# Kernel optimization log

Hardware: AMD Instinct MI355X
Metric: run time of the kernel (lower is better)

Reference implementation:

```python
import jax, jax.numpy as jnp
import numpy as np

B, L = 512, 61440
E_MAX = 128          # max events per window (padded)
THRESHOLD = 0.5      # prob -> binary threshold
IOU_THR = 0.2        # IoU match threshold
LEN_THR = 128        # int(freq*time) = int(256*0.5)


def setup_inputs() -> dict:
    key = jax.random.key(0)
    k1, k2 = jax.random.split(key)
    # block-structured signals -> realistic long, sparse events
    out_blocks = jax.random.uniform(k1, (B, L // 256), dtype=jnp.float32)
    output = jnp.repeat(out_blocks, 256, axis=1)            # [B, L] probs
    tgt_blocks = (jax.random.uniform(k2, (B, L // 512)) > 0.75).astype(jnp.float32)
    target = jnp.repeat(tgt_blocks, 512, axis=1)            # [B, L] binary
    return {"output": output, "target": target}


def _filter_short(b):
    # zero out runs of ones shorter than LEN_THR (ProcessingPostEvent)
    starts = jnp.concatenate([b[:1], ((b[1:] - b[:-1]) == 1).astype(b.dtype)])
    run_id = jnp.cumsum(starts)                              # [L]
    run_len = jax.ops.segment_sum(b, run_id, num_segments=L + 1)
    return b * (run_len[run_id] >= LEN_THR).astype(b.dtype)


def _events(b):
    # binary_to_array: [start, end) pairs, padded to E_MAX with [L, L]
    padded = jnp.concatenate([jnp.zeros(1, b.dtype), b, jnp.zeros(1, b.dtype)])
    d = padded[1:] - padded[:-1]                             # [L+1]
    pos = jnp.arange(L + 1)
    starts = jnp.sort(jnp.where(d == 1, pos, L + 1))[:E_MAX]
    ends = jnp.sort(jnp.where(d == -1, pos, L + 1))[:E_MAX]
    starts = jnp.minimum(starts, L)
    ends = jnp.minimum(ends, L)
    n = (d == 1).sum()
    return starts, ends, n


def _best_match(iou):
    # iou: [E_MAX, E_MAX], invalid entries = -1
    max_col = iou.max(0); idx_col = iou.argmax(0)            # best output row per target col
    max_row = iou.max(1); idx_row = iou.argmax(1)            # best target col per output row
    ar = jnp.arange(E_MAX)
    mutual_row = (idx_col[idx_row] == ar) & (max_row >= IOU_THR)   # [E] rows in mutual match
    mutual_col = (idx_row[idx_col] == ar) & (max_col >= IOU_THR)   # [E] cols in mutual match
    row_one = (~mutual_row) & (max_row >= IOU_THR)
    col_one = (~mutual_col) & (max_col >= IOU_THR)
    onehot_row = (ar[None, :] == idx_row[:, None])           # bm[i, idx_row[i]]
    onehot_col = (ar[:, None] == idx_col[None, :])           # bm[idx_col[j], j]
    ones_m = (onehot_row & row_one[:, None]) | (onehot_col & col_one[None, :])
    kill = mutual_row[:, None] | mutual_col[None, :]         # rows/cols of mutual matches zeroed
    ones_m = ones_m & (~kill)
    tp = mutual_row.sum()                                    # count of '2' marks
    return tp, ones_m


def _per_batch(out_prob, tgt):
    b_out = _filter_short((out_prob >= THRESHOLD).astype(jnp.int32))
    b_tgt = (tgt != 0).astype(jnp.int32)
    s_o, e_o, n_out = _events(b_out)
    s_t, e_t, n_tgt = _events(b_tgt)
    inter = jnp.clip(jnp.minimum(e_o[:, None], e_t[None, :])
                     - jnp.maximum(s_o[:, None], s_t[None, :]), 0)
    la = (e_o - s_o)[:, None]
    lb = (e_t - s_t)[None, :]
    den = jnp.maximum(la + lb - inter, 1)
    valid = (jnp.arange(E_MAX) < n_out)[:, None] & (jnp.arange(E_MAX) < n_tgt)[None, :]
    iou = jnp.where(valid, inter.astype(jnp.float32) / den.astype(jnp.float32), -1.0)
    tp1, ones_m = _best_match(iou)
    # second pass on positions marked '1' (iou elsewhere zeroed in original)
    tp2, _ = _best_match(jnp.where(ones_m, iou, -1.0))
    tp = tp1 + tp2
    t_empty = n_tgt == 0
    o_empty = (~t_empty) & (n_out == 0)
    tp_b = jnp.where(t_empty | o_empty, 0, tp)
    # note: faithful to original (adds output count to FN when target empty, etc.)
    fn_b = jnp.where(t_empty, n_out, jnp.where(o_empty, 0, n_tgt - tp))
    fp_b = jnp.where(t_empty, 0, jnp.where(o_empty, n_tgt, n_out - tp))
    return tp_b, fn_b, fp_b


def reference(output, target):
    tp, fn, fp = jax.vmap(_per_batch)(output, target)
    TP = tp.sum().astype(jnp.float32)
    FN = fn.sum().astype(jnp.float32)
    FP = fp.sum().astype(jnp.float32)
    recall = jnp.where(TP + FN == 0, 0.0, TP / jnp.maximum(TP + FN, 1.0))
    precision = jnp.where(TP + FP == 0, 0.0, TP / jnp.maximum(TP + FP, 1.0))
    f1 = jnp.where(precision + recall == 0, 0.0,
                   2.0 * precision * recall / jnp.maximum(precision + recall, 1e-30))
    return recall, precision, f1
```

## Files before the change

kernel.cpp:

```cpp
#include <hip/hip_runtime.h>

typedef unsigned long long ull;

#define L_LEN 61440
#define NBATCH 512
#define EMAX 128
#define RUNBUF 128
#define NWORDS 960
#define NPADW 1080
#define PADW(w) ((w) + ((w) >> 3))
#define NTHREADS 512
#define IOU_THRESH 0.2f
#define LEN_THRESH 128
#define PADPK 0xF000F000u

__device__ __forceinline__ unsigned int mask16_ge(float4 a, float4 b, float4 c, float4 d, float thr) {
    unsigned int m = 0;
    m |= (a.x >= thr) ? 0x0001u : 0u; m |= (a.y >= thr) ? 0x0002u : 0u;
    m |= (a.z >= thr) ? 0x0004u : 0u; m |= (a.w >= thr) ? 0x0008u : 0u;
    m |= (b.x >= thr) ? 0x0010u : 0u; m |= (b.y >= thr) ? 0x0020u : 0u;
    m |= (b.z >= thr) ? 0x0040u : 0u; m |= (b.w >= thr) ? 0x0080u : 0u;
    m |= (c.x >= thr) ? 0x0100u : 0u; m |= (c.y >= thr) ? 0x0200u : 0u;
    m |= (c.z >= thr) ? 0x0400u : 0u; m |= (c.w >= thr) ? 0x0800u : 0u;
    m |= (d.x >= thr) ? 0x1000u : 0u; m |= (d.y >= thr) ? 0x2000u : 0u;
    m |= (d.z >= thr) ? 0x4000u : 0u; m |= (d.w >= thr) ? 0x8000u : 0u;
    return m;
}

__device__ __forceinline__ unsigned int mask16_ne0(float4 a, float4 b, float4 c, float4 d) {
    unsigned int m = 0;
    m |= (a.x != 0.0f) ? 0x0001u : 0u; m |= (a.y != 0.0f) ? 0x0002u : 0u;
    m |= (a.z != 0.0f) ? 0x0004u : 0u; m |= (a.w != 0.0f) ? 0x0008u : 0u;
    m |= (b.x != 0.0f) ? 0x0010u : 0u; m |= (b.y != 0.0f) ? 0x0020u : 0u;
    m |= (b.z != 0.0f) ? 0x0040u : 0u; m |= (b.w != 0.0f) ? 0x0080u : 0u;
    m |= (c.x != 0.0f) ? 0x0100u : 0u; m |= (c.y != 0.0f) ? 0x0200u : 0u;
    m |= (c.z != 0.0f) ? 0x0400u : 0u; m |= (c.w != 0.0f) ? 0x0800u : 0u;
    m |= (d.x != 0.0f) ? 0x1000u : 0u; m |= (d.y != 0.0f) ? 0x2000u : 0u;
    m |= (d.z != 0.0f) ? 0x4000u : 0u; m |= (d.w != 0.0f) ? 0x8000u : 0u;
    return m;
}

__device__ __forceinline__ float iou_pk(unsigned int pk, int ms, int me, int ml) {
    int s = (int)(pk & 0xffffu), e = (int)(pk >> 16);
    int lo = me < e ? me : e;
    int hi = ms > s ? ms : s;
    int inter = lo - hi; if (inter < 0) inter = 0;
    int den = ml + (e - s) - inter; if (den < 1) den = 1;
    return (float)inter / (float)den;
}

__global__ __launch_bounds__(NTHREADS) void event_f1_kernel(
        const float* __restrict__ outp, const float* __restrict__ tgtp,
        int* __restrict__ counters) {
    __shared__ ull bm[2][NPADW];
    __shared__ int runs_s[2][RUNBUF], runs_e[2][RUNBUF];
    __shared__ int wtot_s[8], wtot_e[8];
    __shared__ __align__(16) unsigned int pse_o[EMAX], pse_t[EMAX];
    __shared__ int idxr[EMAX], idxc[EMAX];
    __shared__ __align__(16) unsigned int rowfl[EMAX], colfl[EMAX];
    __shared__ int n_out_s, n_tgt_s, ftot0, tp_sh;

    const int tid = threadIdx.x;
    const int lane = tid & 63;
    const int wid = tid >> 6;
    const int row = blockIdx.x;

    const float* op = outp + (size_t)row * L_LEN;
    const float* tg = tgtp + (size_t)row * L_LEN;

    if (tid == 0) tp_sh = 0;

    unsigned short* bmo16 = (unsigned short*)bm[0];
    unsigned short* bmt16 = (unsigned short*)bm[1];
    #pragma unroll 2
    for (int it = 0; it < 7; ++it) {
        const float4* po = (const float4*)(op + it * 8192 + tid * 16);
        const float4* pt = (const float4*)(tg + it * 8192 + tid * 16);
        float4 a0 = po[0], a1 = po[1], a2 = po[2], a3 = po[3];
        float4 b0 = pt[0], b1 = pt[1], b2 = pt[2], b3 = pt[3];
        unsigned int mo = mask16_ge(a0, a1, a2, a3, 0.5f);
        unsigned int mt = mask16_ne0(b0, b1, b2, b3);
        unsigned int u = it * 512 + tid;
        unsigned int pu = u + ((u >> 5) << 2);
        bmo16[pu] = (unsigned short)mo;
        bmt16[pu] = (unsigned short)mt;
    }
    if (tid < 256) {
        const float4* po = (const float4*)(op + 57344 + tid * 16);
        const float4* pt = (const float4*)(tg + 57344 + tid * 16);
        float4 a0 = po[0], a1 = po[1], a2 = po[2], a3 = po[3];
        float4 b0 = pt[0], b1 = pt[1], b2 = pt[2], b3 = pt[3];
        unsigned int mo = mask16_ge(a0, a1, a2, a3, 0.5f);
        unsigned int mt = mask16_ne0(b0, b1, b2, b3);
        unsigned int u = 3584 + tid;
        unsigned int pu = u + ((u >> 5) << 2);
        bmo16[pu] = (unsigned short)mo;
        bmt16[pu] = (unsigned short)mt;
    }
    __syncthreads();

    const int group = tid >> 8;
    const int gtid = tid & 255;
    const ull* bmp = bm[group];
    const int w0 = gtid * 4;
    const bool act = (gtid < 240);

    ull swm0 = 0, swm1 = 0, swm2 = 0, swm3 = 0;
    ull ewm0 = 0, ewm1 = 0, ewm2 = 0, ewm3 = 0;
    int cs = 0, ce = 0;
    if (act) {
        ull wm1 = (w0 > 0) ? bmp[PADW(w0 - 1)] : 0ull;
        int p0 = PADW(w0);
        ull a = bmp[p0], b = bmp[p0 + 1], c = bmp[p0 + 2], d = bmp[p0 + 3];
        ull wp4 = (w0 + 4 < NWORDS) ? bmp[PADW(w0 + 4)] : 0ull;
        swm0 = a & ~((a << 1) | (wm1 >> 63)); ewm0 = a & ~((a >> 1) | (b << 63));
        swm1 = b & ~((b << 1) | (a >> 63));   ewm1 = b & ~((b >> 1) | (c << 63));
        swm2 = c & ~((c << 1) | (b >> 63));   ewm2 = c & ~((c >> 1) | (d << 63));
        swm3 = d & ~((d << 1) | (c >> 63));   ewm3 = d & ~((d >> 1) | (wp4 << 63));
        cs = __popcll(swm0) + __popcll(swm1) + __popcll(swm2) + __popcll(swm3);
        ce = __popcll(ewm0) + __popcll(ewm1) + __popcll(ewm2) + __popcll(ewm3);
    }
    int incl_s = cs, incl_e = ce;
    #pragma unroll
    for (int d = 1; d < 64; d <<= 1) {
        int us = __shfl_up(incl_s, d, 64);
        int ue = __shfl_up(incl_e, d, 64);
        if (lane >= d) { incl_s += us; incl_e += ue; }
    }
    if (lane == 63) { wtot_s[wid] = incl_s; wtot_e[wid] = incl_e; }
    __syncthreads();
    int off_s = incl_s - cs, off_e = incl_e - ce;
    for (int wv = (group << 2); wv < wid; ++wv) { off_s += wtot_s[wv]; off_e += wtot_e[wv]; }

    if (act) {
        ull m; int base;
        m = swm0; base = w0 * 64;
        while (m) { int z = __builtin_ctzll(m); if (off_s < RUNBUF) runs_s[group][off_s] = base + z; ++off_s; m &= m - 1; }
        m = swm1; base += 64;
        while (m) { int z = __builtin_ctzll(m); if (off_s < RUNBUF) runs_s[group][off_s] = base + z; ++off_s; m &= m - 1; }
        m = swm2; base += 64;
        while (m) { int z = __builtin_ctzll(m); if (off_s < RUNBUF) runs_s[group][off_s] = base + z; ++off_s; m &= m - 1; }
        m = swm3; base += 64;
        while (m) { int z = __builtin_ctzll(m); if (off_s < RUNBUF) runs_s[group][off_s] = base + z; ++off_s; m &= m - 1; }
        m = ewm0; base = w0 * 64;
        while (m) { int z = __builtin_ctzll(m); if (off_e < RUNBUF) runs_e[group][off_e] = base + z + 1; ++off_e; m &= m - 1; }
        m = ewm1; base += 64;
        while (m) { int z = __builtin_ctzll(m); if (off_e < RUNBUF) runs_e[group][off_e] = base + z + 1; ++off_e; m &= m - 1; }
        m = ewm2; base += 64;
        while (m) { int z = __builtin_ctzll(m); if (off_e < RUNBUF) runs_e[group][off_e] = base + z + 1; ++off_e; m &= m - 1; }
        m = ewm3; base += 64;
        while (m) { int z = __builtin_ctzll(m); if (off_e < RUNBUF) runs_e[group][off_e] = base + z + 1; ++off_e; m &= m - 1; }
    }
    __syncthreads();

    const int nro = wtot_s[0] + wtot_s[1] + wtot_s[2] + wtot_s[3];
    const int nrt = wtot_s[4] + wtot_s[5] + wtot_s[6] + wtot_s[7];

    int keep = 0, fs = 0, fe = 0, fincl = 0;
    if (tid < 128) {
        int lim = nro < RUNBUF ? nro : RUNBUF;
        if (tid < lim) { fs = runs_s[0][tid]; fe = runs_e[0][tid]; keep = (fe - fs) >= LEN_THRESH ? 1 : 0; }
        fincl = keep;
        #pragma unroll
        for (int d = 1; d < 64; d <<= 1) {
            int u = __shfl_up(fincl, d, 64);
            if (lane >= d) fincl += u;
        }
        if (tid == 63) ftot0 = fincl;
    } else if (tid < 256) {
        int k = tid - 128;
        int mc = nrt < EMAX ? nrt : EMAX;
        pse_t[k] = (k < mc) ? ((unsigned)runs_s[1][k] | ((unsigned)runs_e[1][k] << 16)) : PADPK;
        if (k == 0) n_tgt_s = nrt;
    }
    __syncthreads();
    if (tid < 128) {
        int off = fincl - keep + (tid >= 64 ? ftot0 : 0);
        if (keep && off < EMAX) pse_o[off] = (unsigned)fs | ((unsigned)fe << 16);
        if (tid == 127) n_out_s = ftot0 + fincl;
    }
    __syncthreads();
    {
        int mcl = n_out_s < EMAX ? n_out_s : EMAX;
        if (tid < 128 && tid >= mcl) pse_o[tid] = PADPK;
    }
    __syncthreads();

    int ntc = n_tgt_s < EMAX ? n_tgt_s : EMAX;
    int noc = n_out_s < EMAX ? n_out_s : EMAX;
    const int nt4 = (ntc + 3) & ~3;
    const int no4 = (noc + 3) & ~3;

    unsigned mypk = PADPK;
    if (tid < 128) mypk = pse_o[tid];
    else if (tid < 256) mypk = pse_t[tid - 128];
    const int my_s = (int)(mypk & 0xffffu);
    const int my_e = (int)(mypk >> 16);
    const int my_len = my_e - my_s;

    float best = -2.0f; int bi = 0;
    if (tid < 128) {
        for (int j = 0; j < nt4; j += 4) {
            uint4 pk = *(const uint4*)&pse_t[j];
            float v0 = iou_pk(pk.x, my_s, my_e, my_len);
            float v1 = iou_pk(pk.y, my_s, my_e, my_len);
            float v2 = iou_pk(pk.z, my_s, my_e, my_len);
            float v3 = iou_pk(pk.w, my_s, my_e, my_len);
            if (v0 > best) { best = v0; bi = j; }
            if (v1 > best) { best = v1; bi = j + 1; }
            if (v2 > best) { best = v2; bi = j + 2; }
            if (v3 > best) { best = v3; bi = j + 3; }
        }
        idxr[tid] = bi;
    } else if (tid < 256) {
        for (int i = 0; i < no4; i += 4) {
            uint4 pk = *(const uint4*)&pse_o[i];
            float v0 = iou_pk(pk.x, my_s, my_e, my_len);
            float v1 = iou_pk(pk.y, my_s, my_e, my_len);
            float v2 = iou_pk(pk.z, my_s, my_e, my_len);
            float v3 = iou_pk(pk.w, my_s, my_e, my_len);
            if (v0 > best) { best = v0; bi = i; }
            if (v1 > best) { best = v1; bi = i + 1; }
            if (v2 > best) { best = v2; bi = i + 2; }
            if (v3 > best) { best = v3; bi = i + 3; }
        }
        idxc[tid - 128] = bi;
    }
    __syncthreads();

    bool mm = false;
    if (tid < 128) mm = (idxc[bi] == tid) && (best >= IOU_THRESH);
    else if (tid < 256) mm = (idxr[bi] == tid - 128) && (best >= IOU_THRESH);
    if (tid < 128) {
        ull bb = __ballot(mm);
        if (lane == 0) atomicAdd(&tp_sh, (int)__popcll(bb));
    }
    __syncthreads();

    const int bi0 = bi;
    const bool m0 = mm;
    const bool one0 = (!mm) && (best >= IOU_THRESH);
    if (tid < 128)      rowfl[tid] = (unsigned)bi0 | (one0 ? 0x100u : 0u) | (m0 ? 0x200u : 0u);
    else if (tid < 256) colfl[tid - 128] = (unsigned)bi0 | (one0 ? 0x100u : 0u) | (m0 ? 0x200u : 0u);
    __syncthreads();

    best = -2.0f; bi = 0;
    if (tid < 128) {
        const int i = tid;
        for (int j = 0; j < nt4; j += 4) {
            uint4 pk = *(const uint4*)&pse_t[j];
            uint4 fl = *(const uint4*)&colfl[j];
            bool om0 = (((j + 0 == bi0) && one0) || ((i == (int)(fl.x & 0xffu)) && (fl.x & 0x100u))) && !m0 && !(fl.x & 0x200u);
            bool om1 = (((j + 1 == bi0) && one0) || ((i == (int)(fl.y & 0xffu)) && (fl.y & 0x100u))) && !m0 && !(fl.y & 0x200u);
            bool om2 = (((j + 2 == bi0) && one0) || ((i == (int)(fl.z & 0xffu)) && (fl.z & 0x100u))) && !m0 && !(fl.z & 0x200u);
            bool om3 = (((j + 3 == bi0) && one0) || ((i == (int)(fl.w & 0xffu)) && (fl.w & 0x100u))) && !m0 && !(fl.w & 0x200u);
            float v0 = om0 ? iou_pk(pk.x, my_s, my_e, my_len) : -1.0f;
            float v1 = om1 ? iou_pk(pk.y, my_s, my_e, my_len) : -1.0f;
            float v2 = om2 ? iou_pk(pk.z, my_s, my_e, my_len) : -1.0f;
            float v3 = om3 ? iou_pk(pk.w, my_s, my_e, my_len) : -1.0f;
            if (v0 > best) { best = v0; bi = j; }
            if (v1 > best) { best = v1; bi = j + 1; }
            if (v2 > best) { best = v2; bi = j + 2; }
            if (v3 > best) { best = v3; bi = j + 3; }
        }
        idxr[tid] = bi;
    } else if (tid < 256) {
        const int j = tid - 128;
        for (int i = 0; i < no4; i += 4) {
            uint4 pk = *(const uint4*)&pse_o[i];
            uint4 fl = *(const uint4*)&rowfl[i];
            bool om0 = (((j == (int)(fl.x & 0xffu)) && (fl.x & 0x100u)) || ((i + 0 == bi0) && one0)) && !(fl.x & 0x200u) && !m0;
            bool om1 = (((j == (int)(fl.y & 0xffu)) && (fl.y & 0x100u)) || ((i + 1 == bi0) && one0)) && !(fl.y & 0x200u) && !m0;
            bool om2 = (((j == (int)(fl.z & 0xffu)) && (fl.z & 0x100u)) || ((i + 2 == bi0) && one0)) && !(fl.z & 0x200u) && !m0;
            bool om3 = (((j == (int)(fl.w & 0xffu)) && (fl.w & 0x100u)) || ((i + 3 == bi0) && one0)) && !(fl.w & 0x200u) && !m0;
            float v0 = om0 ? iou_pk(pk.x, my_s, my_e, my_len) : -1.0f;
            float v1 = om1 ? iou_pk(pk.y, my_s, my_e, my_len) : -1.0f;
            float v2 = om2 ? iou_pk(pk.z, my_s, my_e, my_len) : -1.0f;
            float v3 = om3 ? iou_pk(pk.w, my_s, my_e, my_len) : -1.0f;
            if (v0 > best) { best = v0; bi = i; }
            if (v1 > best) { best = v1; bi = i + 1; }
            if (v2 > best) { best = v2; bi = i + 2; }
            if (v3 > best) { best = v3; bi = i + 3; }
        }
        idxc[tid - 128] = bi;
    }
    __syncthreads();

    mm = false;
    if (tid < 128) mm = (idxc[bi] == tid) && (best >= IOU_THRESH);
    else if (tid < 256) mm = (idxr[bi] == tid - 128) && (best >= IOU_THRESH);
    if (tid < 128) {
        ull bb = __ballot(mm);
        if (lane == 0) atomicAdd(&tp_sh, (int)__popcll(bb));
    }
    __syncthreads();

    if (tid == 0) {
        int n_out = n_out_s, n_tgt = n_tgt_s, tp = tp_sh;
        int tpb, fnb, fpb;
        if (n_tgt == 0)      { tpb = 0;  fnb = n_out;      fpb = 0; }
        else if (n_out == 0) { tpb = 0;  fnb = 0;          fpb = n_tgt; }
        else                 { tpb = tp; fnb = n_tgt - tp; fpb = n_out - tp; }
        atomicAdd(&counters[0], tpb);
        atomicAdd(&counters[1], fnb);
        atomicAdd(&counters[2], fpb);
    }
}

__global__ void zero_counters(int* c) {
    if (threadIdx.x < 3) c[threadIdx.x] = 0;
}

__global__ void finalize_kernel(const int* __restrict__ c, float* __restrict__ out) {
    float TP = (float)c[0], FN = (float)c[1], FP = (float)c[2];
    float rd = TP + FN;
    float recall = (rd == 0.0f) ? 0.0f : TP / fmaxf(rd, 1.0f);
    float pd = TP + FP;
    float precision = (pd == 0.0f) ? 0.0f : TP / fmaxf(pd, 1.0f);
    float s = precision + recall;
    float f1 = (s == 0.0f) ? 0.0f : 2.0f * precision * recall / fmaxf(s, 1e-30f);
    out[0] = recall; out[1] = precision; out[2] = f1;
}

extern "C" void kernel_launch(void* const* d_in, const int* in_sizes, int n_in,
                              void* d_out, int out_size, void* d_ws, size_t ws_size,
                              hipStream_t stream) {
    const float* outp = (const float*)d_in[0];
    const float* tgtp = (const float*)d_in[1];
    float* res = (float*)d_out;
    int* counters = (int*)d_ws;

    zero_counters<<<1, 64, 0, stream>>>(counters);
    event_f1_kernel<<<NBATCH, NTHREADS, 0, stream>>>(outp, tgtp, counters);
    finalize_kernel<<<1, 1, 0, stream>>>(counters, res);
}
```

Measured before the change: 63.01 us.

## Double block size for load phase and replace atomics with per-row reduction

Raises the block to 1024 threads so each block loads its row in fewer iterations with more memory parallelism, while later phases stay restricted to the first 512 threads. Replaces the global atomic counters and zeroing kernel with per-row result writes plus a 512-thread reduction in the finalize kernel, which removes one launch. In exchange, half the threads sit idle during the later phases and the larger block may lower occupancy.

```diff
diff --git a/kernel.cpp b/kernel.cpp
--- a/kernel.cpp
+++ b/kernel.cpp
@@ -9,7 +9,7 @@
 #define NWORDS 960
 #define NPADW 1080
 #define PADW(w) ((w) + ((w) >> 3))
-#define NTHREADS 512
+#define NTHREADS 1024
 #define IOU_THRESH 0.2f
 #define LEN_THRESH 128
 #define PADPK 0xF000F000u
@@ -51,10 +51,10 @@
 
 __global__ __launch_bounds__(NTHREADS) void event_f1_kernel(
         const float* __restrict__ outp, const float* __restrict__ tgtp,
-        int* __restrict__ counters) {
+        int* __restrict__ per_row) {
     __shared__ ull bm[2][NPADW];
     __shared__ int runs_s[2][RUNBUF], runs_e[2][RUNBUF];
-    __shared__ int wtot_s[8], wtot_e[8];
+    __shared__ int wtot_s[16], wtot_e[16];
     __shared__ __align__(16) unsigned int pse_o[EMAX], pse_t[EMAX];
     __shared__ int idxr[EMAX], idxc[EMAX];
     __shared__ __align__(16) unsigned int rowfl[EMAX], colfl[EMAX];
@@ -72,38 +72,28 @@
 
     unsigned short* bmo16 = (unsigned short*)bm[0];
     unsigned short* bmt16 = (unsigned short*)bm[1];
-    #pragma unroll 2
-    for (int it = 0; it < 7; ++it) {
-        const float4* po = (const float4*)(op + it * 8192 + tid * 16);
-        const float4* pt = (const float4*)(tg + it * 8192 + tid * 16);
+    #pragma unroll 1
+    for (int it = 0; it < 4; ++it) {
+        if (it == 3 && tid >= 768) break;
+        const float4* po = (const float4*)(op + it * 16384 + tid * 16);
+        const float4* pt = (const float4*)(tg + it * 16384 + tid * 16);
         float4 a0 = po[0], a1 = po[1], a2 = po[2], a3 = po[3];
         float4 b0 = pt[0], b1 = pt[1], b2 = pt[2], b3 = pt[3];
         unsigned int mo = mask16_ge(a0, a1, a2, a3, 0.5f);
         unsigned int mt = mask16_ne0(b0, b1, b2, b3);
-        unsigned int u = it * 512 + tid;
+        unsigned int u = it * 1024 + tid;
         unsigned int pu = u + ((u >> 5) << 2);
         bmo16[pu] = (unsigned short)mo;
         bmt16[pu] = (unsigned short)mt;
     }
-    if (tid < 256) {
-        const float4* po = (const float4*)(op + 57344 + tid * 16);
-        const float4* pt = (const float4*)(tg + 57344 + tid * 16);
-        float4 a0 = po[0], a1 = po[1], a2 = po[2], a3 = po[3];
-        float4 b0 = pt[0], b1 = pt[1], b2 = pt[2], b3 = pt[3];
-        unsigned int mo = mask16_ge(a0, a1, a2, a3, 0.5f);
-        unsigned int mt = mask16_ne0(b0, b1, b2, b3);
-        unsigned int u = 3584 + tid;
-        unsigned int pu = u + ((u >> 5) << 2);
-        bmo16[pu] = (unsigned short)mo;
-        bmt16[pu] = (unsigned short)mt;
-    }
     __syncthreads();
 
     const int group = tid >> 8;
+    const int g = group & 1;
     const int gtid = tid & 255;
-    const ull* bmp = bm[group];
+    const ull* bmp = bm[g];
     const int w0 = gtid * 4;
-    const bool act = (gtid < 240);
+    const bool act = (tid < 512) && (gtid < 240);
 
     ull swm0 = 0, swm1 = 0, swm2 = 0, swm3 = 0;
     ull ewm0 = 0, ewm1 = 0, ewm2 = 0, ewm3 = 0;
@@ -130,26 +120,25 @@
     if (lane == 63) { wtot_s[wid] = incl_s; wtot_e[wid] = incl_e; }
     __syncthreads();
     int off_s = incl_s - cs, off_e = incl_e - ce;
-    for (int wv = (group << 2); wv < wid; ++wv) { off_s += wtot_s[wv]; off_e += wtot_e[wv]; }
-
     if (act) {
+        for (int wv = (g << 2); wv < wid; ++wv) { off_s += wtot_s[wv]; off_e += wtot_e[wv]; }
         ull m; int base;
         m = swm0; base = w0 * 64;
-        while (m) { int z = __builtin_ctzll(m); if (off_s < RUNBUF) runs_s[group][off_s] = base + z; ++off_s; m &= m - 1; }
+        while (m) { int z = __builtin_ctzll(m); if (off_s < RUNBUF) runs_s[g][off_s] = base + z; ++off_s; m &= m - 1; }
         m = swm1; base += 64;
-        while (m) { int z = __builtin_ctzll(m); if (off_s < RUNBUF) runs_s[group][off_s] = base + z; ++off_s; m &= m - 1; }
+        while (m) { int z = __builtin_ctzll(m); if (off_s < RUNBUF) runs_s[g][off_s] = base + z; ++off_s; m &= m - 1; }
         m = swm2; base += 64;
-        while (m) { int z = __builtin_ctzll(m); if (off_s < RUNBUF) runs_s[group][off_s] = base + z; ++off_s; m &= m - 1; }
+        while (m) { int z = __builtin_ctzll(m); if (off_s < RUNBUF) runs_s[g][off_s] = base + z; ++off_s; m &= m - 1; }
         m = swm3; base += 64;
-        while (m) { int z = __builtin_ctzll(m); if (off_s < RUNBUF) runs_s[group][off_s] = base + z; ++off_s; m &= m - 1; }
+        while (m) { int z = __builtin_ctzll(m); if (off_s < RUNBUF) runs_s[g][off_s] = base + z; ++off_s; m &= m - 1; }
         m = ewm0; base = w0 * 64;
-        while (m) { int z = __builtin_ctzll(m); if (off_e < RUNBUF) runs_e[group][off_e] = base + z + 1; ++off_e; m &= m - 1; }
+        while (m) { int z = __builtin_ctzll(m); if (off_e < RUNBUF) runs_e[g][off_e] = base + z + 1; ++off_e; m &= m - 1; }
         m = ewm1; base += 64;
-        while (m) { int z = __builtin_ctzll(m); if (off_e < RUNBUF) runs_e[group][off_e] = base + z + 1; ++off_e; m &= m - 1; }
+        while (m) { int z = __builtin_ctzll(m); if (off_e < RUNBUF) runs_e[g][off_e] = base + z + 1; ++off_e; m &= m - 1; }
         m = ewm2; base += 64;
-        while (m) { int z = __builtin_ctzll(m); if (off_e < RUNBUF) runs_e[group][off_e] = base + z + 1; ++off_e; m &= m - 1; }
+        while (m) { int z = __builtin_ctzll(m); if (off_e < RUNBUF) runs_e[g][off_e] = base + z + 1; ++off_e; m &= m - 1; }
         m = ewm3; base += 64;
-        while (m) { int z = __builtin_ctzll(m); if (off_e < RUNBUF) runs_e[group][off_e] = base + z + 1; ++off_e; m &= m - 1; }
+        while (m) { int z = __builtin_ctzll(m); if (off_e < RUNBUF) runs_e[g][off_e] = base + z + 1; ++off_e; m &= m - 1; }
     }
     __syncthreads();
 
@@ -301,25 +290,42 @@
         if (n_tgt == 0)      { tpb = 0;  fnb = n_out;      fpb = 0; }
         else if (n_out == 0) { tpb = 0;  fnb = 0;          fpb = n_tgt; }
         else                 { tpb = tp; fnb = n_tgt - tp; fpb = n_out - tp; }
-        atomicAdd(&counters[0], tpb);
-        atomicAdd(&counters[1], fnb);
-        atomicAdd(&counters[2], fpb);
-    }
-}
-
-__global__ void zero_counters(int* c) {
-    if (threadIdx.x < 3) c[threadIdx.x] = 0;
-}
-
-__global__ void finalize_kernel(const int* __restrict__ c, float* __restrict__ out) {
-    float TP = (float)c[0], FN = (float)c[1], FP = (float)c[2];
-    float rd = TP + FN;
-    float recall = (rd == 0.0f) ? 0.0f : TP / fmaxf(rd, 1.0f);
-    float pd = TP + FP;
-    float precision = (pd == 0.0f) ? 0.0f : TP / fmaxf(pd, 1.0f);
-    float s = precision + recall;
-    float f1 = (s == 0.0f) ? 0.0f : 2.0f * precision * recall / fmaxf(s, 1e-30f);
-    out[0] = recall; out[1] = precision; out[2] = f1;
+        per_row[row * 3 + 0] = tpb;
+        per_row[row * 3 + 1] = fnb;
+        per_row[row * 3 + 2] = fpb;
+    }
+}
+
+__global__ __launch_bounds__(512) void finalize_kernel(const int* __restrict__ per_row,
+                                                       float* __restrict__ out) {
+    __shared__ int sm[3][8];
+    const int tid = threadIdx.x;
+    const int lane = tid & 63;
+    const int wid = tid >> 6;
+    int tp = per_row[tid * 3 + 0];
+    int fn = per_row[tid * 3 + 1];
+    int fp = per_row[tid * 3 + 2];
+    #pragma unroll
+    for (int d = 32; d > 0; d >>= 1) {
+        tp += __shfl_down(tp, d, 64);
+        fn += __shfl_down(fn, d, 64);
+        fp += __shfl_down(fp, d, 64);
+    }
+    if (lane == 0) { sm[0][wid] = tp; sm[1][wid] = fn; sm[2][wid] = fp; }
+    __syncthreads();
+    if (tid == 0) {
+        int TPi = 0, FNi = 0, FPi = 0;
+        #pragma unroll
+        for (int w = 0; w < 8; ++w) { TPi += sm[0][w]; FNi += sm[1][w]; FPi += sm[2][w]; }
+        float TP = (float)TPi, FN = (float)FNi, FP = (float)FPi;
+        float rd = TP + FN;
+        float recall = (rd == 0.0f) ? 0.0f : TP / fmaxf(rd, 1.0f);
+        float pd = TP + FP;
+        float precision = (pd == 0.0f) ? 0.0f : TP / fmaxf(pd, 1.0f);
+        float s = precision + recall;
+        float f1 = (s == 0.0f) ? 0.0f : 2.0f * precision * recall / fmaxf(s, 1e-30f);
+        out[0] = recall; out[1] = precision; out[2] = f1;
+    }
 }
 
 extern "C" void kernel_launch(void* const* d_in, const int* in_sizes, int n_in,
@@ -328,9 +334,8 @@
     const float* outp = (const float*)d_in[0];
     const float* tgtp = (const float*)d_in[1];
     float* res = (float*)d_out;
-    int* counters = (int*)d_ws;
-
-    zero_counters<<<1, 64, 0, stream>>>(counters);
-    event_f1_kernel<<<NBATCH, NTHREADS, 0, stream>>>(outp, tgtp, counters);
-    finalize_kernel<<<1, 1, 0, stream>>>(counters, res);
-}
+    int* per_row = (int*)d_ws;
+
+    event_f1_kernel<<<NBATCH, NTHREADS, 0, stream>>>(outp, tgtp, per_row);
+    finalize_kernel<<<1, 512, 0, stream>>>(per_row, res);
+}
```

Result: faster. 57.49 us (-8.8%).
